# Optimization experiments

Measured on AMD Instinct MI355X. Metric: run time of the kernel, lower is better.

The kernel has to match this reference:

```python
import jax, jax.numpy as jnp
import numpy as np

B, T, D, L = 16, 4096, 512, 1024

def setup_inputs() -> dict:
    key = jax.random.key(0)
    k1, k2, k3, k4 = jax.random.split(key, 4)
    x = jax.random.normal(k1, (B, T, D), dtype=jnp.float32)
    q = jax.random.normal(k2, (L, D), dtype=jnp.float32)
    fc_w = jax.random.normal(k3, (1, D), dtype=jnp.float32) * (1.0 / np.sqrt(D))
    fc_b = jax.random.normal(k4, (1,), dtype=jnp.float32) * 0.01
    return {"x": x, "q": q, "fc_w": fc_w, "fc_b": fc_b}

def reference(x, q, fc_w, fc_b):
    # att: (B, T, L) label-wise attention scores, softmax over sequence axis T
    att = jnp.einsum('btd,ld->btl', x, q)
    att = jax.nn.softmax(att, axis=1)
    # out: (B, L, D) attention-pooled features per label
    out = jnp.einsum('btl,btd->bld', att, x)
    # linear head to scalar per label -> (B, L)
    return jnp.einsum('bld,od->blo', out, fc_w).squeeze(-1) + fc_b[0]
```

## Files before the change

### kernel.cpp

```cpp
#include <hip/hip_runtime.h>

#define B_ 16
#define T_ 4096
#define D_ 512
#define L_ 1024
#define NTCH 32
#define PPLANE ((size_t)B_ * NTCH * L_)
#define XBLK (B_ * T_ / 16)

typedef _Float16 half8 __attribute__((ext_vector_type(8)));
typedef float float4v __attribute__((ext_vector_type(4)));

__device__ inline void gl_lds(const void* g, void* l) {
    __builtin_amdgcn_global_load_lds(
        (const __attribute__((address_space(1))) unsigned int*)g,
        (__attribute__((address_space(3))) unsigned int*)l, 16, 0, 0);
}

__global__ __launch_bounds__(256) void k_prep(const float* __restrict__ x,
                                              const float* __restrict__ q,
                                              const float* __restrict__ w,
                                              _Float16* __restrict__ xt,
                                              _Float16* __restrict__ qt,
                                              float* __restrict__ y) {
    __shared__ float Xl[16 * 512];
    __shared__ float Yp[64];
    const int tid = threadIdx.x;
    const bool isq = blockIdx.x >= XBLK;
    const int blk = isq ? (blockIdx.x - XBLK) : blockIdx.x;
    const float* bsrc = (isq ? q : x) + (size_t)blk * (16 * 512);
    half8* dst = (half8*)(isq ? qt : xt) + (size_t)blk * 1024;

#pragma unroll
    for (int it = 0; it < 8; ++it) {
        int f = it * 1024 + tid * 4;
        int row = f >> 9, k = f & 511;
        int pc = (k >> 2) ^ (row & 7);
        *(float4*)&Xl[row * 512 + pc * 4] = *(const float4*)(bsrc + f);
    }
    __syncthreads();

    const int wv = tid >> 6, lane = tid & 63;
    const int row = lane & 15, gq = lane >> 4;
    float acc = 0.f;
#pragma unroll
    for (int it = 0; it < 4; ++it) {
        int kc = it * 4 + wv;
        int c0 = kc * 8 + gq * 2;
        int k0 = kc * 32 + gq * 8;
        float4 a = *(const float4*)&Xl[row * 512 + ((c0 ^ (row & 7)) << 2)];
        float4 c = *(const float4*)&Xl[row * 512 + (((c0 + 1) ^ (row & 7)) << 2)];
        half8 h;
        h[0] = (_Float16)a.x; h[1] = (_Float16)a.y; h[2] = (_Float16)a.z; h[3] = (_Float16)a.w;
        h[4] = (_Float16)c.x; h[5] = (_Float16)c.y; h[6] = (_Float16)c.z; h[7] = (_Float16)c.w;
        dst[kc * 64 + lane] = h;
        if (!isq) {
            float4 wa = *(const float4*)(w + k0);
            float4 wc = *(const float4*)(w + k0 + 4);
            acc = fmaf(a.x, wa.x, acc); acc = fmaf(a.y, wa.y, acc);
            acc = fmaf(a.z, wa.z, acc); acc = fmaf(a.w, wa.w, acc);
            acc = fmaf(c.x, wc.x, acc); acc = fmaf(c.y, wc.y, acc);
            acc = fmaf(c.z, wc.z, acc); acc = fmaf(c.w, wc.w, acc);
        }
    }
    if (!isq) {
        acc += __shfl_xor(acc, 16, 64);
        acc += __shfl_xor(acc, 32, 64);
        if (gq == 0) Yp[wv * 16 + row] = acc;
        __syncthreads();
        if (tid < 16)
            y[blk * 16 + tid] = Yp[tid] + Yp[16 + tid] + Yp[32 + tid] + Yp[48 + tid];
    }
}

__global__ __launch_bounds__(256, 2) void k_mfma(const _Float16* __restrict__ xt,
                                                 const _Float16* __restrict__ qt,
                                                 const float* __restrict__ y,
                                                 float* __restrict__ part) {
    __shared__ half8 S[3072];
    __shared__ float ys[256];

    const int bid  = blockIdx.x;
    const int xcd  = bid & 7;
    const int jj   = bid >> 3;
    const int tile = (xcd << 5) | (jj >> 3);
    const int lblk = jj & 7;
    const int tblk = tile & 15;
    const int b    = tile >> 4;

    const int tid  = threadIdx.x;
    const int lane = tid & 63;
    const int w    = tid >> 6;
    const int wt   = w >> 1, wl = w & 1;
    const int tb0  = b * (T_ / 16) + tblk * 16;
    const int lb0  = lblk * 8;

    ys[tid] = y[(size_t)b * T_ + tblk * 256 + tid];

    float4v acc[8][4];
#pragma unroll
    for (int i = 0; i < 8; ++i)
#pragma unroll
        for (int j = 0; j < 4; ++j) acc[i][j] = (float4v){0.f, 0.f, 0.f, 0.f};

    const half8* Xg = (const half8*)xt;
    const half8* Qg = (const half8*)qt;

    for (int kk = 0; kk < D_ / 64; ++kk) {
        __syncthreads();
#pragma unroll
        for (int s = 0; s < 2; ++s) {
            const int kc = kk * 2 + s;
#pragma unroll
            for (int p = 0; p < 4; ++p) {
                int xb = p * 4 + w;
                gl_lds(Xg + ((size_t)(tb0 + xb) * (D_ / 32) + kc) * 64 + lane,
                       &S[s * 1536 + xb * 64]);
            }
#pragma unroll
            for (int p = 0; p < 2; ++p) {
                int qb = p * 4 + w;
                gl_lds(Qg + ((size_t)(lb0 + qb) * (D_ / 32) + kc) * 64 + lane,
                       &S[s * 1536 + 1024 + qb * 64]);
            }
        }
        __syncthreads();

#pragma unroll
        for (int s = 0; s < 2; ++s) {
            half8 A[8], Bv[4];
#pragma unroll
            for (int i = 0; i < 8; ++i) A[i] = S[s * 1536 + (wt * 8 + i) * 64 + lane];
#pragma unroll
            for (int j = 0; j < 4; ++j) Bv[j] = S[s * 1536 + 1024 + (wl * 4 + j) * 64 + lane];
#pragma unroll
            for (int i = 0; i < 8; ++i)
#pragma unroll
                for (int j = 0; j < 4; ++j)
                    acc[i][j] = __builtin_amdgcn_mfma_f32_16x16x32_f16(A[i], Bv[j], acc[i][j], 0, 0, 0);
        }
    }

    const int quad = lane >> 4, cl = lane & 15;
    const int tchunk = tblk * 2 + wt;
    const int lbase  = lblk * 128 + wl * 64;

    float* pm = part;
    float* pz = part + PPLANE;
    float* pn = part + 2 * PPLANE;

#pragma unroll
    for (int j = 0; j < 4; ++j) {
        float m = -1e30f;
#pragma unroll
        for (int i = 0; i < 8; ++i)
#pragma unroll
            for (int r = 0; r < 4; ++r) m = fmaxf(m, acc[i][j][r]);
        float z = 0.f, n = 0.f;
#pragma unroll
        for (int i = 0; i < 8; ++i)
#pragma unroll
            for (int r = 0; r < 4; ++r) {
                float p = __expf(acc[i][j][r] - m);
                z += p;
                n = fmaf(p, ys[wt * 128 + i * 16 + quad * 4 + r], n);
            }
#pragma unroll
        for (int msk = 16; msk <= 32; msk <<= 1) {
            float om = __shfl_xor(m, msk, 64);
            float oz = __shfl_xor(z, msk, 64);
            float on = __shfl_xor(n, msk, 64);
            float mn = fmaxf(m, om);
            float s0 = __expf(m - mn), s1 = __expf(om - mn);
            z = fmaf(z, s0, oz * s1);
            n = fmaf(n, s0, on * s1);
            m = mn;
        }
        if (quad == 0) {
            int l = lbase + j * 16 + cl;
            size_t a = ((size_t)b * NTCH + tchunk) * L_ + l;
            pm[a] = m;
            pz[a] = z;
            pn[a] = n;
        }
    }
}

__global__ __launch_bounds__(256) void k_comb_p(const float* __restrict__ part,
                                                const float* __restrict__ fc_b,
                                                float* __restrict__ out) {
    int bl = blockIdx.x * 256 + threadIdx.x;
    int b = bl >> 10, l = bl & (L_ - 1);
    const float* pm = part;
    const float* pz = part + PPLANE;
    const float* pn = part + 2 * PPLANE;
    float m = -1e30f, z = 0.f, n = 0.f;
    for (int c = 0; c < NTCH; ++c) {
        size_t a = ((size_t)b * NTCH + c) * L_ + l;
        float pmv = pm[a], pzv = pz[a], pnv = pn[a];
        float mn = fmaxf(m, pmv);
        float s0 = __expf(m - mn), s1 = __expf(pmv - mn);
        z = fmaf(z, s0, pzv * s1);
        n = fmaf(n, s0, pnv * s1);
        m = mn;
    }
    out[bl] = n / z + fc_b[0];
}

#define NC 8
#define TC (T_ / NC)
#define BT 128
#define BL 128
#define KK 32

__global__ __launch_bounds__(256) void k_y(const float* __restrict__ x,
                                           const float* __restrict__ w,
                                           float* __restrict__ y) {
    int row  = (blockIdx.x * 256 + threadIdx.x) >> 6;
    int lane = threadIdx.x & 63;
    const float* r = x + (size_t)row * D_;
    float s = 0.f;
#pragma unroll
    for (int k = 0; k < D_; k += 64) s = fmaf(r[k + lane], w[k + lane], s);
#pragma unroll
    for (int o = 32; o > 0; o >>= 1) s += __shfl_xor(s, o, 64);
    if (lane == 0) y[row] = s;
}

__global__ __launch_bounds__(256, 2) void k_main(const float* __restrict__ x,
                                                 const float* __restrict__ q,
                                                 const float* __restrict__ y,
                                                 float* __restrict__ part) {
    __shared__ float Xs[KK][BT + 4];
    __shared__ float Qs[KK][BL + 4];
    const int tid = threadIdx.x;
    const int ty = tid & 15, tx = tid >> 4;
    const int lb = blockIdx.x * BL, chunk = blockIdx.y, b = blockIdx.z;
    const int g = tid & 7, r0 = tid >> 3;

    float run_m[8], run_z[8], run_n[8];
#pragma unroll
    for (int j = 0; j < 8; ++j) { run_m[j] = -1e30f; run_z[j] = 0.f; run_n[j] = 0.f; }

    for (int tt = 0; tt < TC; tt += BT) {
        const int t0 = chunk * TC + tt;
        float s[8][8];
#pragma unroll
        for (int i = 0; i < 8; ++i)
#pragma unroll
            for (int j = 0; j < 8; ++j) s[i][j] = 0.f;
        for (int kc = 0; kc < D_; kc += KK) {
            __syncthreads();
#pragma unroll
            for (int p = 0; p < 4; ++p) {
                int rr = p * 32 + r0;
                float4 vx = *(const float4*)(x + ((size_t)b * T_ + t0 + rr) * D_ + kc + g * 4);
                float4 vq = *(const float4*)(q + (size_t)(lb + rr) * D_ + kc + g * 4);
                Xs[g * 4 + 0][rr] = vx.x; Xs[g * 4 + 1][rr] = vx.y;
                Xs[g * 4 + 2][rr] = vx.z; Xs[g * 4 + 3][rr] = vx.w;
                Qs[g * 4 + 0][rr] = vq.x; Qs[g * 4 + 1][rr] = vq.y;
                Qs[g * 4 + 2][rr] = vq.z; Qs[g * 4 + 3][rr] = vq.w;
            }
            __syncthreads();
#pragma unroll
            for (int k = 0; k < KK; ++k) {
                float4 a0 = *(const float4*)&Xs[k][ty * 4];
                float4 a1 = *(const float4*)&Xs[k][64 + ty * 4];
                float4 b0 = *(const float4*)&Qs[k][tx * 4];
                float4 b1 = *(const float4*)&Qs[k][64 + tx * 4];
                float av[8] = {a0.x, a0.y, a0.z, a0.w, a1.x, a1.y, a1.z, a1.w};
                float bv[8] = {b0.x, b0.y, b0.z, b0.w, b1.x, b1.y, b1.z, b1.w};
#pragma unroll
                for (int i = 0; i < 8; ++i)
#pragma unroll
                    for (int j = 0; j < 8; ++j) s[i][j] = fmaf(av[i], bv[j], s[i][j]);
            }
        }
        float yv[8];
#pragma unroll
        for (int i = 0; i < 8; ++i) {
            int tl = (i < 4) ? (ty * 4 + i) : (64 + ty * 4 + (i - 4));
            yv[i] = y[(size_t)b * T_ + t0 + tl];
        }
#pragma unroll
        for (int j = 0; j < 8; ++j) {
            float mt = s[0][j];
#pragma unroll
            for (int i = 1; i < 8; ++i) mt = fmaxf(mt, s[i][j]);
            float mn = fmaxf(run_m[j], mt);
            float sc = __expf(run_m[j] - mn);
            float z = run_z[j] * sc, n = run_n[j] * sc;
#pragma unroll
            for (int i = 0; i < 8; ++i) {
                float p = __expf(s[i][j] - mn);
                z += p;
                n = fmaf(p, yv[i], n);
            }
            run_m[j] = mn; run_z[j] = z; run_n[j] = n;
        }
    }
#pragma unroll
    for (int msk = 1; msk < 16; msk <<= 1) {
#pragma unroll
        for (int j = 0; j < 8; ++j) {
            float om = __shfl_xor(run_m[j], msk, 64);
            float oz = __shfl_xor(run_z[j], msk, 64);
            float on = __shfl_xor(run_n[j], msk, 64);
            float mn = fmaxf(run_m[j], om);
            float s0 = __expf(run_m[j] - mn), s1 = __expf(om - mn);
            run_z[j] = fmaf(run_z[j], s0, oz * s1);
            run_n[j] = fmaf(run_n[j], s0, on * s1);
            run_m[j] = mn;
        }
    }
    if (ty == 0) {
#pragma unroll
        for (int j = 0; j < 8; ++j) {
            int ll = (j < 4) ? (tx * 4 + j) : (64 + tx * 4 + (j - 4));
            size_t idx = ((size_t)(b * L_ + lb + ll) * NC + chunk) * 3;
            part[idx + 0] = run_m[j];
            part[idx + 1] = run_z[j];
            part[idx + 2] = run_n[j];
        }
    }
}

__global__ __launch_bounds__(256) void k_comb_f(const float* __restrict__ part,
                                                const float* __restrict__ fc_b,
                                                float* __restrict__ out) {
    int bl = blockIdx.x * 256 + threadIdx.x;
    float m = -1e30f, z = 0.f, n = 0.f;
    for (int c = 0; c < NC; ++c) {
        size_t idx = ((size_t)bl * NC + c) * 3;
        float pm = part[idx + 0], pz = part[idx + 1], pn = part[idx + 2];
        float mn = fmaxf(m, pm);
        float s0 = __expf(m - mn), s1 = __expf(pm - mn);
        z = fmaf(z, s0, pz * s1);
        n = fmaf(n, s0, pn * s1);
        m = mn;
    }
    out[bl] = n / z + fc_b[0];
}

extern "C" void kernel_launch(void* const* d_in, const int* in_sizes, int n_in,
                              void* d_out, int out_size, void* d_ws, size_t ws_size,
                              hipStream_t stream) {
    const float* x    = (const float*)d_in[0];
    const float* q    = (const float*)d_in[1];
    const float* fc_w = (const float*)d_in[2];
    const float* fc_b = (const float*)d_in[3];
    float* out = (float*)d_out;
    float* ws  = (float*)d_ws;

    const size_t Y_F    = (size_t)B_ * T_;
    const size_t PART_F = 3 * PPLANE;
    const size_t PARTF_FALLBACK = (size_t)B_ * L_ * NC * 3;
    const size_t XT_H   = (size_t)B_ * T_ * D_;
    const size_t QT_H   = (size_t)L_ * D_;
    const size_t need   = (Y_F + PART_F) * 4 + (XT_H + QT_H) * 2;

    if (ws_size >= need) {
        float* y    = ws;
        float* part = ws + Y_F;
        _Float16* xt = (_Float16*)(ws + Y_F + PART_F);
        _Float16* qt = xt + XT_H;
        k_prep<<<XBLK + L_ / 16, 256, 0, stream>>>(x, q, fc_w, xt, qt, y);
        k_mfma<<<2048, 256, 0, stream>>>(xt, qt, y, part);
        k_comb_p<<<B_ * L_ / 256, 256, 0, stream>>>(part, fc_b, out);
    } else {
        float* y    = ws;
        float* part = ws + Y_F;
        (void)PARTF_FALLBACK;
        k_y   <<<B_ * T_ / 4, 256, 0, stream>>>(x, fc_w, y);
        k_main<<<dim3(L_ / BL, NC, B_), 256, 0, stream>>>(x, q, y, part);
        k_comb_f<<<B_ * L_ / 256, 256, 0, stream>>>(part, fc_b, out);
    }
}
```

Measured before the change: 277.4 us.

## Fuse x fp32-to-fp16 conversion into MFMA kernel, drop staged xt buffer

The separate prep pass that wrote a full fp16 copy of x is removed. The MFMA kernel now loads fp32 x directly, converts it in registers and stores it to a padded LDS tile, while q is converted by a small standalone kernel and y is computed by a vectorized row-dot kernel. This avoids writing and rereading a 64 MB fp16 intermediate. In exchange, each MFMA block reads twice the bytes of x per tile and x is reloaded by all 8 L-blocks as fp32, and the synchronous register-path load replaces the async global_load_lds path for x.

Result: slower. 285.4 us (+2.9%).

```diff
diff --git a/kernel.cpp b/kernel.cpp
--- a/kernel.cpp
+++ b/kernel.cpp
@@ -6,9 +6,9 @@
 #define L_ 1024
 #define NTCH 32
 #define PPLANE ((size_t)B_ * NTCH * L_)
-#define XBLK (B_ * T_ / 16)
 
 typedef _Float16 half8 __attribute__((ext_vector_type(8)));
+typedef _Float16 h4_t  __attribute__((ext_vector_type(4)));
 typedef float float4v __attribute__((ext_vector_type(4)));
 
 __device__ inline void gl_lds(const void* g, void* l) {
@@ -17,67 +17,45 @@
         (__attribute__((address_space(3))) unsigned int*)l, 16, 0, 0);
 }
 
-__global__ __launch_bounds__(256) void k_prep(const float* __restrict__ x,
-                                              const float* __restrict__ q,
-                                              const float* __restrict__ w,
-                                              _Float16* __restrict__ xt,
-                                              _Float16* __restrict__ qt,
-                                              float* __restrict__ y) {
-    __shared__ float Xl[16 * 512];
-    __shared__ float Yp[64];
-    const int tid = threadIdx.x;
-    const bool isq = blockIdx.x >= XBLK;
-    const int blk = isq ? (blockIdx.x - XBLK) : blockIdx.x;
-    const float* bsrc = (isq ? q : x) + (size_t)blk * (16 * 512);
-    half8* dst = (half8*)(isq ? qt : xt) + (size_t)blk * 1024;
-
-#pragma unroll
-    for (int it = 0; it < 8; ++it) {
-        int f = it * 1024 + tid * 4;
-        int row = f >> 9, k = f & 511;
-        int pc = (k >> 2) ^ (row & 7);
-        *(float4*)&Xl[row * 512 + pc * 4] = *(const float4*)(bsrc + f);
-    }
-    __syncthreads();
-
-    const int wv = tid >> 6, lane = tid & 63;
-    const int row = lane & 15, gq = lane >> 4;
-    float acc = 0.f;
-#pragma unroll
-    for (int it = 0; it < 4; ++it) {
-        int kc = it * 4 + wv;
-        int c0 = kc * 8 + gq * 2;
-        int k0 = kc * 32 + gq * 8;
-        float4 a = *(const float4*)&Xl[row * 512 + ((c0 ^ (row & 7)) << 2)];
-        float4 c = *(const float4*)&Xl[row * 512 + (((c0 + 1) ^ (row & 7)) << 2)];
-        half8 h;
-        h[0] = (_Float16)a.x; h[1] = (_Float16)a.y; h[2] = (_Float16)a.z; h[3] = (_Float16)a.w;
-        h[4] = (_Float16)c.x; h[5] = (_Float16)c.y; h[6] = (_Float16)c.z; h[7] = (_Float16)c.w;
-        dst[kc * 64 + lane] = h;
-        if (!isq) {
-            float4 wa = *(const float4*)(w + k0);
-            float4 wc = *(const float4*)(w + k0 + 4);
-            acc = fmaf(a.x, wa.x, acc); acc = fmaf(a.y, wa.y, acc);
-            acc = fmaf(a.z, wa.z, acc); acc = fmaf(a.w, wa.w, acc);
-            acc = fmaf(c.x, wc.x, acc); acc = fmaf(c.y, wc.y, acc);
-            acc = fmaf(c.z, wc.z, acc); acc = fmaf(c.w, wc.w, acc);
-        }
-    }
-    if (!isq) {
-        acc += __shfl_xor(acc, 16, 64);
-        acc += __shfl_xor(acc, 32, 64);
-        if (gq == 0) Yp[wv * 16 + row] = acc;
-        __syncthreads();
-        if (tid < 16)
-            y[blk * 16 + tid] = Yp[tid] + Yp[16 + tid] + Yp[32 + tid] + Yp[48 + tid];
-    }
-}
-
-__global__ __launch_bounds__(256, 2) void k_mfma(const _Float16* __restrict__ xt,
+__global__ __launch_bounds__(256) void k_y(const float* __restrict__ x,
+                                           const float* __restrict__ w,
+                                           float* __restrict__ y) {
+    int row  = blockIdx.x * 4 + (threadIdx.x >> 6);
+    int lane = threadIdx.x & 63;
+    const float4* r = (const float4*)(x + (size_t)row * D_);
+    const float4* wv = (const float4*)w;
+    float4 a = r[lane], b = r[lane + 64];
+    float4 wa = wv[lane], wb = wv[lane + 64];
+    float s = a.x * wa.x;
+    s = fmaf(a.y, wa.y, s); s = fmaf(a.z, wa.z, s); s = fmaf(a.w, wa.w, s);
+    s = fmaf(b.x, wb.x, s); s = fmaf(b.y, wb.y, s);
+    s = fmaf(b.z, wb.z, s); s = fmaf(b.w, wb.w, s);
+#pragma unroll
+    for (int o = 32; o > 0; o >>= 1) s += __shfl_xor(s, o, 64);
+    if (lane == 0) y[row] = s;
+}
+
+__global__ __launch_bounds__(256) void k_qcvt(const float* __restrict__ src,
+                                              _Float16* __restrict__ dst) {
+    int idx = blockIdx.x * 256 + threadIdx.x;
+    int g   = idx & 63;
+    int row = idx >> 6;
+    const float* p = src + (size_t)row * D_ + g * 8;
+    float4 a = *(const float4*)p;
+    float4 c = *(const float4*)(p + 4);
+    half8 h;
+    h[0] = (_Float16)a.x; h[1] = (_Float16)a.y; h[2] = (_Float16)a.z; h[3] = (_Float16)a.w;
+    h[4] = (_Float16)c.x; h[5] = (_Float16)c.y; h[6] = (_Float16)c.z; h[7] = (_Float16)c.w;
+    size_t blk = (size_t)(row >> 4) * (D_ / 32) + (g >> 2);
+    ((half8*)dst)[blk * 64 + (row & 15) + 16 * (g & 3)] = h;
+}
+
+__global__ __launch_bounds__(256, 2) void k_mfma(const float* __restrict__ x,
                                                  const _Float16* __restrict__ qt,
                                                  const float* __restrict__ y,
                                                  float* __restrict__ part) {
-    __shared__ half8 S[3072];
+    __shared__ _Float16 Sx[256 * 72];
+    __shared__ half8 Sq[1024];
     __shared__ float ys[256];
 
     const int bid  = blockIdx.x;
@@ -92,7 +70,7 @@
     const int lane = tid & 63;
     const int w    = tid >> 6;
     const int wt   = w >> 1, wl = w & 1;
-    const int tb0  = b * (T_ / 16) + tblk * 16;
+    const int rq   = lane >> 4, ch = lane & 15;
     const int lb0  = lblk * 8;
 
     ys[tid] = y[(size_t)b * T_ + tblk * 256 + tid];
@@ -103,26 +81,23 @@
 #pragma unroll
         for (int j = 0; j < 4; ++j) acc[i][j] = (float4v){0.f, 0.f, 0.f, 0.f};
 
-    const half8* Xg = (const half8*)xt;
     const half8* Qg = (const half8*)qt;
+    const float* xb = x + ((size_t)b * T_ + tblk * 256) * D_;
 
     for (int kk = 0; kk < D_ / 64; ++kk) {
         __syncthreads();
 #pragma unroll
-        for (int s = 0; s < 2; ++s) {
-            const int kc = kk * 2 + s;
-#pragma unroll
-            for (int p = 0; p < 4; ++p) {
-                int xb = p * 4 + w;
-                gl_lds(Xg + ((size_t)(tb0 + xb) * (D_ / 32) + kc) * 64 + lane,
-                       &S[s * 1536 + xb * 64]);
-            }
-#pragma unroll
-            for (int p = 0; p < 2; ++p) {
-                int qb = p * 4 + w;
-                gl_lds(Qg + ((size_t)(lb0 + qb) * (D_ / 32) + kc) * 64 + lane,
-                       &S[s * 1536 + 1024 + qb * 64]);
-            }
+        for (int p = 0; p < 4; ++p) {
+            int u = p * 4 + w;
+            gl_lds(Qg + ((size_t)(lb0 + (u & 7)) * (D_ / 32) + kk * 2 + (u >> 3)) * 64 + lane,
+                   &Sq[u * 64]);
+        }
+#pragma unroll
+        for (int it = 0; it < 16; ++it) {
+            int row = w * 64 + it * 4 + rq;
+            float4 a = *(const float4*)(xb + (size_t)row * D_ + kk * 64 + ch * 4);
+            h4_t h = {(_Float16)a.x, (_Float16)a.y, (_Float16)a.z, (_Float16)a.w};
+            *(h4_t*)&Sx[row * 72 + ch * 4] = h;
         }
         __syncthreads();
 
@@ -130,9 +105,11 @@
         for (int s = 0; s < 2; ++s) {
             half8 A[8], Bv[4];
 #pragma unroll
-            for (int i = 0; i < 8; ++i) A[i] = S[s * 1536 + (wt * 8 + i) * 64 + lane];
-#pragma unroll
-            for (int j = 0; j < 4; ++j) Bv[j] = S[s * 1536 + 1024 + (wl * 4 + j) * 64 + lane];
+            for (int i = 0; i < 8; ++i)
+                A[i] = *(const half8*)&Sx[(wt * 128 + i * 16 + ch) * 72 + s * 32 + rq * 8];
+#pragma unroll
+            for (int j = 0; j < 4; ++j)
+                Bv[j] = Sq[((u_int32_t)s * 8 + wl * 4 + j) * 64 + lane];
 #pragma unroll
             for (int i = 0; i < 8; ++i)
 #pragma unroll
@@ -213,20 +190,6 @@
 #define BL 128
 #define KK 32
 
-__global__ __launch_bounds__(256) void k_y(const float* __restrict__ x,
-                                           const float* __restrict__ w,
-                                           float* __restrict__ y) {
-    int row  = (blockIdx.x * 256 + threadIdx.x) >> 6;
-    int lane = threadIdx.x & 63;
-    const float* r = x + (size_t)row * D_;
-    float s = 0.f;
-#pragma unroll
-    for (int k = 0; k < D_; k += 64) s = fmaf(r[k + lane], w[k + lane], s);
-#pragma unroll
-    for (int o = 32; o > 0; o >>= 1) s += __shfl_xor(s, o, 64);
-    if (lane == 0) y[row] = s;
-}
-
 __global__ __launch_bounds__(256, 2) void k_main(const float* __restrict__ x,
                                                  const float* __restrict__ q,
                                                  const float* __restrict__ y,
@@ -354,23 +317,20 @@
 
     const size_t Y_F    = (size_t)B_ * T_;
     const size_t PART_F = 3 * PPLANE;
-    const size_t PARTF_FALLBACK = (size_t)B_ * L_ * NC * 3;
-    const size_t XT_H   = (size_t)B_ * T_ * D_;
     const size_t QT_H   = (size_t)L_ * D_;
-    const size_t need   = (Y_F + PART_F) * 4 + (XT_H + QT_H) * 2;
+    const size_t need   = (Y_F + PART_F) * 4 + QT_H * 2;
 
     if (ws_size >= need) {
         float* y    = ws;
         float* part = ws + Y_F;
-        _Float16* xt = (_Float16*)(ws + Y_F + PART_F);
-        _Float16* qt = xt + XT_H;
-        k_prep<<<XBLK + L_ / 16, 256, 0, stream>>>(x, q, fc_w, xt, qt, y);
-        k_mfma<<<2048, 256, 0, stream>>>(xt, qt, y, part);
+        _Float16* qt = (_Float16*)(ws + Y_F + PART_F);
+        k_y   <<<B_ * T_ / 4, 256, 0, stream>>>(x, fc_w, y);
+        k_qcvt<<<(L_ * 64) / 256, 256, 0, stream>>>(q, qt);
+        k_mfma<<<2048, 256, 0, stream>>>(x, qt, y, part);
         k_comb_p<<<B_ * L_ / 256, 256, 0, stream>>>(part, fc_b, out);
     } else {
         float* y    = ws;
         float* part = ws + Y_F;
-        (void)PARTF_FALLBACK;
         k_y   <<<B_ * T_ / 4, 256, 0, stream>>>(x, fc_w, y);
         k_main<<<dim3(L_ / BL, NC, B_), 256, 0, stream>>>(x, q, y, part);
         k_comb_f<<<B_ * L_ / 256, 256, 0, stream>>>(part, fc_b, out);
```
